# Performance work log

Hardware: AMD Instinct MI355X
Metric: run time of the kernel (lower is better)

The kernel has to match this reference:

```python
import jax, jax.numpy as jnp
import numpy as np

N_ATOMS = 16384
N_BLOCKS = 4096
K = 3          # top-k nearest context atoms (min(3, n_ctx) in original; n_ctx >> 3 here)
EPS_W = 1e-8   # inverse-distance weight epsilon (matches original)
EPS_D = 1e-12  # tiny epsilon inside sqrt for numerical safety of the distance


def setup_inputs() -> dict:
    key = jax.random.key(0)
    k1, k2, k3, k4, k5 = jax.random.split(key, 5)
    # coordinates spread out like real molecular coords (Angstrom-ish scale)
    X = jax.random.normal(k1, (N_ATOMS, 3), dtype=jnp.float32) * 10.0
    base_noise = jax.random.normal(k2, (N_ATOMS, 3), dtype=jnp.float32)      # randn_like(X)
    centroid_noise = jax.random.normal(k3, (N_ATOMS, 3), dtype=jnp.float32)  # per-atom randn(3)
    block_ids = jnp.sort(jax.random.randint(k4, (N_ATOMS,), 0, N_BLOCKS)).astype(jnp.int32)
    generate_mask = jax.random.randint(k5, (N_BLOCKS,), 0, 2).astype(bool)
    return {
        "X": X,
        "base_noise": base_noise,
        "centroid_noise": centroid_noise,
        "block_ids": block_ids,
        "generate_mask": generate_mask,
    }


def reference(X, base_noise, centroid_noise, block_ids, generate_mask):
    """Vectorized sample_chemical_prior: for every generated atom, find the 3
    nearest CONTEXT atoms, take an inverse-distance-weighted centroid, and add
    0.5 * gaussian noise. Non-generated atoms keep base_noise (randn_like)."""
    n = X.shape[0]
    gen_atoms = generate_mask[block_ids]           # [N] atoms being generated
    ctx = ~gen_atoms                               # [N] context atoms

    # pairwise squared distances via ||a||^2 + ||b||^2 - 2 a.b  -> [N, N]
    xn = jnp.sum(X * X, axis=-1)
    sq = xn[:, None] + xn[None, :] - 2.0 * (X @ X.T)
    d = jnp.sqrt(jnp.maximum(sq, 0.0) + EPS_D)

    # only context atoms are valid neighbor candidates; exclude self for safety
    not_self = ~jnp.eye(n, dtype=bool)
    d = jnp.where(ctx[None, :] & not_self, d, jnp.inf)

    # k nearest context atoms per row (smallest distances)
    neg_dk, idx = jax.lax.top_k(-d, K)             # [N, K]
    dk = -neg_dk

    # inverse-distance weights, normalized (matches original)
    w = 1.0 / (dk + EPS_W)
    w = w / jnp.sum(w, axis=-1, keepdims=True)

    coords = X[idx]                                # [N, K, 3] gather neighbor coords
    centroid = jnp.sum(coords * w[..., None], axis=1)  # [N, 3]

    x0 = jnp.where(gen_atoms[:, None], centroid + 0.5 * centroid_noise, base_noise)
    return x0
```

## Files before the change

### kernel.cpp

```cpp
#include <hip/hip_runtime.h>
#include <cstdint>

#define N_ATOMS 16384
#define NBLK 64
#define NTHR 256
#define G 24
#define NCELLS 13824
#define NCELLS_PAD 14336
#define CPT 14
#define BOX_LO -48.0f
#define INV_CELL 0.25f
#define SINIT 3.0e38f

#define OFF_COUNTS 0
#define OFF_BLKGEN 256
#define OFF_BLKGOFF 512
#define OFF_FLAGS 1024
#define OFF_CNT 3072
#define OFF_START 60416
#define OFF_GENIDX 118016
#define OFF_CTX4 183552

__device__ __forceinline__ int cell1(float x) {
    int c = (int)floorf((x - BOX_LO) * INV_CELL);
    return min(max(c, 0), G - 1);
}

__device__ __forceinline__ void ins3(float v, int vi,
                                     float& s1, float& s2, float& s3,
                                     int& i1, int& i2, int& i3)
{
    const bool b1 = v < s1, b2 = v < s2, b3 = v < s3;
    s3 = b2 ? s2 : (b3 ? v : s3);   i3 = b2 ? i2 : (b3 ? vi : i3);
    s2 = b1 ? s1 : (b2 ? v : s2);   i2 = b1 ? i1 : (b2 ? vi : i2);
    s1 = b1 ? v : s1;               i1 = b1 ? vi : i1;
}

__device__ __forceinline__ void ins3v(float v, float& s1, float& s2, float& s3)
{
    const bool b1 = v < s1, b2 = v < s2, b3 = v < s3;
    s3 = b2 ? s2 : (b3 ? v : s3);
    s2 = b1 ? s1 : (b2 ? v : s2);
    s1 = b1 ? v : s1;
}

__global__ __launch_bounds__(256)
void k0_zero(int4* __restrict__ cell_cnt4)
{
    cell_cnt4[blockIdx.x * 256 + threadIdx.x] = make_int4(0, 0, 0, 0);
}

__global__ __launch_bounds__(NTHR)
void k1_classify(const float* __restrict__ X,
                 const int* __restrict__ block_ids,
                 const unsigned int* __restrict__ mask,
                 const float* __restrict__ base_noise,
                 float* __restrict__ out,
                 unsigned long long* __restrict__ flags,
                 int* __restrict__ blk_gen,
                 int* __restrict__ cell_cnt)
{
    __shared__ int sflag;
    __shared__ int wg[4];
    const int t = threadIdx.x;
    const int wave = t >> 6, lane = t & 63;

    if (t == 0) sflag = 0;
    __syncthreads();
    if (mask[t] > 1u) sflag = 1;
    __syncthreads();
    const bool is_u8 = (sflag != 0);
    const unsigned char* m8 = (const unsigned char*)mask;

    const int i = blockIdx.x * NTHR + t;
    const int bid = block_ids[i];
    const bool g = is_u8 ? (m8[bid] != 0) : (mask[bid] != 0u);

    out[3 * i + 0] = base_noise[3 * i + 0];
    out[3 * i + 1] = base_noise[3 * i + 1];
    out[3 * i + 2] = base_noise[3 * i + 2];

    const unsigned long long mg = __ballot(g);
    if (lane == 0) { flags[blockIdx.x * 4 + wave] = mg; wg[wave] = __popcll(mg); }
    __syncthreads();
    if (t == 0) blk_gen[blockIdx.x] = wg[0] + wg[1] + wg[2] + wg[3];

    if (!g) {
        const float x = X[3 * i], y = X[3 * i + 1], z = X[3 * i + 2];
        const int cx = cell1(x), cy = cell1(y), cz = cell1(z);
        atomicAdd(&cell_cnt[(cz * G + cy) * G + cx], 1);
    }
}

__global__ __launch_bounds__(1024)
void k2_scan(int* __restrict__ cell_cnt,
             int* __restrict__ cell_start,
             const int* __restrict__ blk_gen,
             int* __restrict__ blk_goff,
             int* __restrict__ counts)
{
    const int t = threadIdx.x;
    const int wave = t >> 6, lane = t & 63;
    int loc[CPT]; int sum = 0;
    #pragma unroll
    for (int k = 0; k < CPT; ++k) {
        const int v = cell_cnt[t * CPT + k];
        loc[k] = sum; sum += v;
    }
    int v = sum;
    #pragma unroll
    for (int d = 1; d < 64; d <<= 1) { const int u = __shfl_up(v, d); if (lane >= d) v += u; }
    __shared__ int wsum[16], wexc[16];
    if (lane == 63) wsum[wave] = v;
    __syncthreads();
    if (t < 16) {
        int v2 = wsum[t];
        const int orig = v2;
        #pragma unroll
        for (int d = 1; d < 16; d <<= 1) { const int u = __shfl_up(v2, d); if (t >= d) v2 += u; }
        wexc[t] = v2 - orig;
    }
    __syncthreads();
    const int base = wexc[wave] + (v - sum);
    #pragma unroll
    for (int k = 0; k < CPT; ++k) {
        cell_start[t * CPT + k] = base + loc[k];
        cell_cnt[t * CPT + k] = 0;
    }
    if (t == 1023) cell_start[NCELLS_PAD] = base + sum;
    __syncthreads();
    if (t < 64) {
        const int o = blk_gen[t];
        int s = o;
        #pragma unroll
        for (int d = 1; d < 64; d <<= 1) { const int u = __shfl_up(s, d); if (t >= d) s += u; }
        blk_goff[t] = s - o;
        if (t == 63) { counts[1] = s; counts[0] = N_ATOMS - s; }
    }
}

__global__ __launch_bounds__(NTHR)
void k3_scatter(const float* __restrict__ X,
                const unsigned long long* __restrict__ flags,
                const int* __restrict__ blk_goff,
                const int* __restrict__ cell_start,
                int* __restrict__ cell_cur,
                float4* __restrict__ ctx4s,
                int* __restrict__ genidx)
{
    const int t = threadIdx.x;
    const int wave = t >> 6, lane = t & 63;
    const int i = blockIdx.x * NTHR + t;
    const unsigned long long fw = flags[blockIdx.x * 4 + wave];
    const bool g = (fw >> lane) & 1ull;
    int og = blk_goff[blockIdx.x];
    int oc = blockIdx.x * NTHR - og;
    #pragma unroll
    for (int w = 0; w < 4; ++w) {
        if (w < wave) {
            const int p = __popcll(flags[blockIdx.x * 4 + w]);
            og += p; oc += 64 - p;
        }
    }
    const unsigned long long below = (1ull << lane) - 1ull;
    og += __popcll(fw & below);
    oc += __popcll((~fw) & below);
    if (g) {
        genidx[og] = i;
    } else {
        const float x = X[3 * i], y = X[3 * i + 1], z = X[3 * i + 2];
        float xn = x * x; xn += y * y; xn += z * z;
        const int cx = cell1(x), cy = cell1(y), cz = cell1(z);
        const int c = (cz * G + cy) * G + cx;
        const int pos = cell_start[c] + atomicAdd(&cell_cur[c], 1);
        ctx4s[pos] = make_float4(x, y, z, xn);
    }
}

__global__ __launch_bounds__(512)
void k4_search(const float* __restrict__ X,
               const float* __restrict__ cnoise,
               const int* __restrict__ counts,
               const int* __restrict__ cell_start,
               const float4* __restrict__ ctx4s,
               const int* __restrict__ genidx,
               float* __restrict__ out)
{
    const int n_gen = counts[1];
    const int wave = threadIdx.x >> 6, lane = threadIdx.x & 63;
    const int slot = (int)blockIdx.x * 8 + wave;
    if (slot >= n_gen) return;

    const int ai = genidx[slot];
    const float qx = X[3 * ai], qy = X[3 * ai + 1], qz = X[3 * ai + 2];
    float xnq = qx * qx; xnq += qy * qy; xnq += qz * qz;
    const int cqx = cell1(qx), cqy = cell1(qy), cqz = cell1(qz);

    float s1 = SINIT, s2 = SINIT, s3 = SINIT;
    int i1 = 0, i2 = 0, i3 = 0;

    {
        int st = 0, cnt = 0;
        if (lane < 9) {
            const int dy = lane % 3 - 1, dz = lane / 3 - 1;
            const int cy = cqy + dy, cz = cqz + dz;
            if ((unsigned)cy < G && (unsigned)cz < G) {
                const int xlo = max(cqx - 1, 0), xhi = min(cqx + 1, G - 1);
                const int c0 = (cz * G + cy) * G + xlo;
                st = cell_start[c0];
                cnt = cell_start[c0 + (xhi - xlo + 1)] - st;
            }
        }
        int stv[9], base[10];
        base[0] = 0;
        #pragma unroll
        for (int k = 0; k < 9; ++k) {
            stv[k] = __builtin_amdgcn_readlane(st, k);
            base[k + 1] = base[k] + __builtin_amdgcn_readlane(cnt, k);
        }
        const int T = base[9];
        const int nro = (T + 63) >> 6;
        if (nro > 0) {
            auto calcP = [&](int j) -> int {
                const int jc = min(j, T - 1);
                int p = stv[0] + jc;
                #pragma unroll
                for (int k = 1; k < 9; ++k)
                    p = (jc >= base[k]) ? stv[k] + (jc - base[k]) : p;
                return p;
            };
            int p0 = calcP(lane);
            float4 cc0 = ctx4s[p0];
            for (int ro = 0; ro < nro; ++ro) {
                int p1 = p0; float4 cc1 = cc0;
                if (ro + 1 < nro) { p1 = calcP((ro + 1) * 64 + lane); cc1 = ctx4s[p1]; }
                if (ro * 64 + lane < T) {
                    const float dot = qx * cc0.x + qy * cc0.y + qz * cc0.z;
                    const float sq = (xnq + cc0.w) - 2.0f * dot;
                    ins3(sq, p0, s1, s2, s3, i1, i2, i3);
                }
                p0 = p1; cc0 = cc1;
            }
        }
    }

    auto converged = [&](float bnd) -> bool {
        const int c = __popcll(__ballot(s1 + 0.01f < bnd))
                    + __popcll(__ballot(s2 + 0.01f < bnd))
                    + __popcll(__ballot(s3 + 0.01f < bnd));
        return c >= 3;
    };

    bool done = converged(16.0f);

    if (!done) {
        auto searchOwner = [&](int ebase_r, int jc) -> int {
            int L = 0;
            #pragma unroll
            for (int stp = 32; stp >= 1; stp >>= 1) {
                const int cand = L + stp;
                const int bv = __shfl(ebase_r, cand);
                if (bv <= jc) L = cand;
            }
            return L;
        };
        auto flatScan = [&](int T, int ebase_r, int pk_r) {
            const int iters = (T + 63) >> 6;
            if (iters == 0) return;
            int jc0 = min(lane, T - 1);
            int p0 = __shfl(pk_r, searchOwner(ebase_r, jc0)) + jc0;
            float4 cc0 = ctx4s[p0];
            for (int it = 0; it < iters; ++it) {
                int p1 = p0; float4 cc1 = cc0;
                if (it + 1 < iters) {
                    const int jc1 = min((it + 1) * 64 + lane, T - 1);
                    p1 = __shfl(pk_r, searchOwner(ebase_r, jc1)) + jc1;
                    cc1 = ctx4s[p1];
                }
                if (it * 64 + lane < T) {
                    const float dot = qx * cc0.x + qy * cc0.y + qz * cc0.z;
                    const float sq = (xnq + cc0.w) - 2.0f * dot;
                    ins3(sq, p0, s1, s2, s3, i1, i2, i3);
                }
                p0 = p1; cc0 = cc1;
            }
        };
        auto prefixT = [&](int cnt, int& ebase_r, int& T) {
            int pre = cnt;
            #pragma unroll
            for (int d = 1; d < 64; d <<= 1) {
                const int u = __shfl_up(pre, d);
                if (lane >= d) pre += u;
            }
            T = __shfl(pre, 63);
            ebase_r = pre - cnt;
        };
        auto ringScan = [&](int P, int R) {
            const int B = 2 * R + 1;
            const int NR = B * B;
            const int NS = 2 * NR;
            auto segRange = [&](int u, int& st, int& cnt) {
                st = 0; cnt = 0;
                if (u >= NS) return;
                const int side = (u >= NR) ? 1 : 0;
                const int v = side ? u - NR : u;
                const int dy = v % B - R, dz = v / B - R;
                const int cy = cqy + dy, cz = cqz + dz;
                if ((unsigned)cy >= G || (unsigned)cz >= G) return;
                const bool inner = max(abs(dy), abs(dz)) <= P;
                int xlo, xhi;
                if (inner) {
                    if (side) { xlo = cqx + P + 1; xhi = cqx + R; }
                    else      { xlo = cqx - R;     xhi = cqx - P - 1; }
                } else {
                    if (side) return;
                    xlo = cqx - R; xhi = cqx + R;
                }
                xlo = max(xlo, 0); xhi = min(xhi, G - 1);
                if (xlo > xhi) return;
                const int c0 = (cz * G + cy) * G + xlo;
                st = cell_start[c0];
                cnt = cell_start[c0 + (xhi - xlo + 1)] - st;
            };
            const int nro = (NS + 63) >> 6;
            int st0, c0r;
            segRange(lane, st0, c0r);
            for (int ro = 0; ro < nro; ++ro) {
                int st1 = st0, c1r = c0r;
                if (ro + 1 < nro) segRange((ro + 1) * 64 + lane, st1, c1r);
                int eb, Tr;
                prefixT(c0r, eb, Tr);
                if (Tr > 0) flatScan(Tr, eb, st0 - eb);
                st0 = st1; c0r = c1r;
            }
        };

        #pragma unroll
        for (int li = 1; li < 4; ++li) {
            if (!done) {
                const int R = 1 << li;
                ringScan(1 << (li - 1), R);
                done = converged((float)(4 * R) * (float)(4 * R));
            }
        }
        if (!done) {
            s1 = SINIT; s2 = SINIT; s3 = SINIT;
            i1 = 0; i2 = 0; i3 = 0;
            const int n_ctx = counts[0];
            for (int base = 0; base < n_ctx; base += 64) {
                const int p = base + lane;
                if (p < n_ctx) {
                    const float4 cc = ctx4s[p];
                    const float dot = qx * cc.x + qy * cc.y + qz * cc.z;
                    const float sq = (xnq + cc.w) - 2.0f * dot;
                    ins3(sq, p, s1, s2, s3, i1, i2, i3);
                }
            }
        }
    }

    #pragma unroll
    for (int m = 1; m < 64; m <<= 1) {
        const float a = __shfl_xor(s1, m); const int ja = __shfl_xor(i1, m);
        const float b = __shfl_xor(s2, m); const int jb = __shfl_xor(i2, m);
        const float c = __shfl_xor(s3, m); const int jc = __shfl_xor(i3, m);
        ins3(a, ja, s1, s2, s3, i1, i2, i3);
        ins3(b, jb, s1, s2, s3, i1, i2, i3);
        ins3(c, jc, s1, s2, s3, i1, i2, i3);
    }

    if (lane == 0) {
        const float d1 = sqrtf(fmaxf(s1, 0.0f) + 1e-12f);
        const float d2 = sqrtf(fmaxf(s2, 0.0f) + 1e-12f);
        const float d3 = sqrtf(fmaxf(s3, 0.0f) + 1e-12f);
        float w1 = 1.0f / (d1 + 1e-8f);
        float w2 = 1.0f / (d2 + 1e-8f);
        float w3 = 1.0f / (d3 + 1e-8f);
        float wsum = w1 + w2;
        wsum += w3;
        w1 /= wsum; w2 /= wsum; w3 /= wsum;
        const float4 c1 = ctx4s[i1];
        const float4 c2 = ctx4s[i2];
        const float4 c3 = ctx4s[i3];
        float cxo = w1 * c1.x + w2 * c2.x; cxo += w3 * c3.x;
        float cyo = w1 * c1.y + w2 * c2.y; cyo += w3 * c3.y;
        float czo = w1 * c1.z + w2 * c2.z; czo += w3 * c3.z;
        out[3 * ai + 0] = cxo + 0.5f * cnoise[3 * ai + 0];
        out[3 * ai + 1] = cyo + 0.5f * cnoise[3 * ai + 1];
        out[3 * ai + 2] = czo + 0.5f * cnoise[3 * ai + 2];
    }
}

extern "C" void kernel_launch(void* const* d_in, const int* in_sizes, int n_in,
                              void* d_out, int out_size, void* d_ws, size_t ws_size,
                              hipStream_t stream) {
    const float* X          = (const float*)d_in[0];
    const float* base_noise = (const float*)d_in[1];
    const float* cnoise     = (const float*)d_in[2];
    const int*   block_ids  = (const int*)d_in[3];
    const unsigned int* gmask = (const unsigned int*)d_in[4];
    float* out = (float*)d_out;

    char* ws = (char*)d_ws;
    int*    counts     = (int*)(ws + OFF_COUNTS);
    int*    blk_gen    = (int*)(ws + OFF_BLKGEN);
    int*    blk_goff   = (int*)(ws + OFF_BLKGOFF);
    unsigned long long* flags = (unsigned long long*)(ws + OFF_FLAGS);
    int*    cell_cnt   = (int*)(ws + OFF_CNT);
    int*    cell_start = (int*)(ws + OFF_START);
    int*    genidx     = (int*)(ws + OFF_GENIDX);
    float4* ctx4s      = (float4*)(ws + OFF_CTX4);

    k0_zero<<<NCELLS_PAD / 1024, 256, 0, stream>>>((int4*)cell_cnt);
    k1_classify<<<NBLK, NTHR, 0, stream>>>(X, block_ids, gmask, base_noise,
                                           out, flags, blk_gen, cell_cnt);
    k2_scan<<<1, 1024, 0, stream>>>(cell_cnt, cell_start, blk_gen, blk_goff, counts);
    k3_scatter<<<NBLK, NTHR, 0, stream>>>(X, flags, blk_goff, cell_start,
                                          cell_cnt, ctx4s, genidx);
    k4_search<<<N_ATOMS / 8, 512, 0, stream>>>(X, cnoise, counts, cell_start,
                                               ctx4s, genidx, out);
}
```

Before: 50.65 us.

## Move cell histogram into shared-memory sort kernel and drop zero kernel

The classify kernel now writes a 16-bit cell id per atom instead of doing global atomics. The single-block scan kernel builds the histogram, prefix sum and per-atom slot positions with shared-memory atomics, so the separate zeroing kernel goes away and the scatter kernel no longer needs global atomics. The search kernel moves to 256-thread blocks with an early exit, and the ring enumeration now covers only the non-empty shell segments instead of testing and rejecting half the lanes. The cost is that one 1024-thread block now processes all 16K atoms serially, in two passes.

```diff
diff --git a/kernel.cpp b/kernel.cpp
--- a/kernel.cpp
+++ b/kernel.cpp
@@ -16,10 +16,11 @@
 #define OFF_BLKGEN 256
 #define OFF_BLKGOFF 512
 #define OFF_FLAGS 1024
-#define OFF_CNT 3072
-#define OFF_START 60416
-#define OFF_GENIDX 118016
-#define OFF_CTX4 183552
+#define OFF_ACELL 3072
+#define OFF_POS 35840
+#define OFF_START 101376
+#define OFF_GENIDX 158976
+#define OFF_CTX4 224512
 
 __device__ __forceinline__ int cell1(float x) {
     int c = (int)floorf((x - BOX_LO) * INV_CELL);
@@ -36,20 +37,6 @@
     s1 = b1 ? v : s1;               i1 = b1 ? vi : i1;
 }
 
-__device__ __forceinline__ void ins3v(float v, float& s1, float& s2, float& s3)
-{
-    const bool b1 = v < s1, b2 = v < s2, b3 = v < s3;
-    s3 = b2 ? s2 : (b3 ? v : s3);
-    s2 = b1 ? s1 : (b2 ? v : s2);
-    s1 = b1 ? v : s1;
-}
-
-__global__ __launch_bounds__(256)
-void k0_zero(int4* __restrict__ cell_cnt4)
-{
-    cell_cnt4[blockIdx.x * 256 + threadIdx.x] = make_int4(0, 0, 0, 0);
-}
-
 __global__ __launch_bounds__(NTHR)
 void k1_classify(const float* __restrict__ X,
                  const int* __restrict__ block_ids,
@@ -58,7 +45,7 @@
                  float* __restrict__ out,
                  unsigned long long* __restrict__ flags,
                  int* __restrict__ blk_gen,
-                 int* __restrict__ cell_cnt)
+                 unsigned short* __restrict__ acell)
 {
     __shared__ int sflag;
     __shared__ int wg[4];
@@ -85,32 +72,47 @@
     __syncthreads();
     if (t == 0) blk_gen[blockIdx.x] = wg[0] + wg[1] + wg[2] + wg[3];
 
+    unsigned short c = 0xFFFFu;
     if (!g) {
         const float x = X[3 * i], y = X[3 * i + 1], z = X[3 * i + 2];
-        const int cx = cell1(x), cy = cell1(y), cz = cell1(z);
-        atomicAdd(&cell_cnt[(cz * G + cy) * G + cx], 1);
-    }
+        c = (unsigned short)((cell1(z) * G + cell1(y)) * G + cell1(x));
+    }
+    acell[i] = c;
 }
 
 __global__ __launch_bounds__(1024)
-void k2_scan(int* __restrict__ cell_cnt,
+void k2_sort(const unsigned short* __restrict__ acell,
              int* __restrict__ cell_start,
+             int* __restrict__ pos,
              const int* __restrict__ blk_gen,
              int* __restrict__ blk_goff,
              int* __restrict__ counts)
 {
+    __shared__ int hist[NCELLS_PAD];
+    __shared__ int wsum[16], wexc[16];
     const int t = threadIdx.x;
     const int wave = t >> 6, lane = t & 63;
+
+    #pragma unroll
+    for (int k = 0; k < CPT; ++k) hist[t * CPT + k] = 0;
+    __syncthreads();
+
+    #pragma unroll
+    for (int it = 0; it < N_ATOMS / 1024; ++it) {
+        const unsigned short c = acell[it * 1024 + t];
+        if (c != 0xFFFFu) atomicAdd(&hist[c], 1);
+    }
+    __syncthreads();
+
     int loc[CPT]; int sum = 0;
     #pragma unroll
     for (int k = 0; k < CPT; ++k) {
-        const int v = cell_cnt[t * CPT + k];
+        const int v = hist[t * CPT + k];
         loc[k] = sum; sum += v;
     }
     int v = sum;
     #pragma unroll
     for (int d = 1; d < 64; d <<= 1) { const int u = __shfl_up(v, d); if (lane >= d) v += u; }
-    __shared__ int wsum[16], wexc[16];
     if (lane == 63) wsum[wave] = v;
     __syncthreads();
     if (t < 16) {
@@ -124,11 +126,20 @@
     const int base = wexc[wave] + (v - sum);
     #pragma unroll
     for (int k = 0; k < CPT; ++k) {
-        cell_start[t * CPT + k] = base + loc[k];
-        cell_cnt[t * CPT + k] = 0;
+        const int st = base + loc[k];
+        cell_start[t * CPT + k] = st;
+        hist[t * CPT + k] = st;
     }
     if (t == 1023) cell_start[NCELLS_PAD] = base + sum;
     __syncthreads();
+
+    #pragma unroll
+    for (int it = 0; it < N_ATOMS / 1024; ++it) {
+        const int i = it * 1024 + t;
+        const unsigned short c = acell[i];
+        if (c != 0xFFFFu) pos[i] = atomicAdd(&hist[c], 1);
+    }
+
     if (t < 64) {
         const int o = blk_gen[t];
         int s = o;
@@ -143,8 +154,7 @@
 void k3_scatter(const float* __restrict__ X,
                 const unsigned long long* __restrict__ flags,
                 const int* __restrict__ blk_goff,
-                const int* __restrict__ cell_start,
-                int* __restrict__ cell_cur,
+                const int* __restrict__ pos,
                 float4* __restrict__ ctx4s,
                 int* __restrict__ genidx)
 {
@@ -153,31 +163,23 @@
     const int i = blockIdx.x * NTHR + t;
     const unsigned long long fw = flags[blockIdx.x * 4 + wave];
     const bool g = (fw >> lane) & 1ull;
-    int og = blk_goff[blockIdx.x];
-    int oc = blockIdx.x * NTHR - og;
-    #pragma unroll
-    for (int w = 0; w < 4; ++w) {
-        if (w < wave) {
-            const int p = __popcll(flags[blockIdx.x * 4 + w]);
-            og += p; oc += 64 - p;
-        }
-    }
-    const unsigned long long below = (1ull << lane) - 1ull;
-    og += __popcll(fw & below);
-    oc += __popcll((~fw) & below);
     if (g) {
+        int og = blk_goff[blockIdx.x];
+        #pragma unroll
+        for (int w = 0; w < 4; ++w) {
+            if (w < wave) og += __popcll(flags[blockIdx.x * 4 + w]);
+        }
+        const unsigned long long below = (1ull << lane) - 1ull;
+        og += __popcll(fw & below);
         genidx[og] = i;
     } else {
         const float x = X[3 * i], y = X[3 * i + 1], z = X[3 * i + 2];
         float xn = x * x; xn += y * y; xn += z * z;
-        const int cx = cell1(x), cy = cell1(y), cz = cell1(z);
-        const int c = (cz * G + cy) * G + cx;
-        const int pos = cell_start[c] + atomicAdd(&cell_cur[c], 1);
-        ctx4s[pos] = make_float4(x, y, z, xn);
-    }
-}
-
-__global__ __launch_bounds__(512)
+        ctx4s[pos[i]] = make_float4(x, y, z, xn);
+    }
+}
+
+__global__ __launch_bounds__(NTHR)
 void k4_search(const float* __restrict__ X,
                const float* __restrict__ cnoise,
                const int* __restrict__ counts,
@@ -188,7 +190,8 @@
 {
     const int n_gen = counts[1];
     const int wave = threadIdx.x >> 6, lane = threadIdx.x & 63;
-    const int slot = (int)blockIdx.x * 8 + wave;
+    if ((int)blockIdx.x * 4 >= n_gen) return;
+    const int slot = (int)blockIdx.x * 4 + wave;
     if (slot >= n_gen) return;
 
     const int ai = genidx[slot];
@@ -297,25 +300,35 @@
         };
         auto ringScan = [&](int P, int R) {
             const int B = 2 * R + 1;
-            const int NR = B * B;
-            const int NS = 2 * NR;
+            const int RP = R - P;
+            const int PP = 2 * P + 1;
+            const int A = 2 * RP * B;
+            const int C = PP * 2 * RP;
+            const int NS = A + C + 2 * PP * PP;
             auto segRange = [&](int u, int& st, int& cnt) {
                 st = 0; cnt = 0;
                 if (u >= NS) return;
-                const int side = (u >= NR) ? 1 : 0;
-                const int v = side ? u - NR : u;
-                const int dy = v % B - R, dz = v / B - R;
+                int dy, dz, xlo, xhi;
+                if (u < A) {
+                    const int q = u / B, rdy = u - q * B;
+                    dz = (q < RP) ? (-R + q) : (P + 1 + (q - RP));
+                    dy = rdy - R;
+                    xlo = cqx - R; xhi = cqx + R;
+                } else if (u < A + C) {
+                    const int v = u - A, W = 2 * RP;
+                    const int q = v / W, w = v - q * W;
+                    dz = -P + q;
+                    dy = (w < RP) ? (-R + w) : (P + 1 + (w - RP));
+                    xlo = cqx - R; xhi = cqx + R;
+                } else {
+                    const int v = u - A - C;
+                    const int side = v & 1, v2 = v >> 1;
+                    dy = v2 % PP - P; dz = v2 / PP - P;
+                    if (side) { xlo = cqx + P + 1; xhi = cqx + R; }
+                    else      { xlo = cqx - R;     xhi = cqx - P - 1; }
+                }
                 const int cy = cqy + dy, cz = cqz + dz;
                 if ((unsigned)cy >= G || (unsigned)cz >= G) return;
-                const bool inner = max(abs(dy), abs(dz)) <= P;
-                int xlo, xhi;
-                if (inner) {
-                    if (side) { xlo = cqx + P + 1; xhi = cqx + R; }
-                    else      { xlo = cqx - R;     xhi = cqx - P - 1; }
-                } else {
-                    if (side) return;
-                    xlo = cqx - R; xhi = cqx + R;
-                }
                 xlo = max(xlo, 0); xhi = min(xhi, G - 1);
                 if (xlo > xhi) return;
                 const int c0 = (cz * G + cy) * G + xlo;
@@ -406,17 +419,16 @@
     int*    blk_gen    = (int*)(ws + OFF_BLKGEN);
     int*    blk_goff   = (int*)(ws + OFF_BLKGOFF);
     unsigned long long* flags = (unsigned long long*)(ws + OFF_FLAGS);
-    int*    cell_cnt   = (int*)(ws + OFF_CNT);
+    unsigned short* acell = (unsigned short*)(ws + OFF_ACELL);
+    int*    pos        = (int*)(ws + OFF_POS);
     int*    cell_start = (int*)(ws + OFF_START);
     int*    genidx     = (int*)(ws + OFF_GENIDX);
     float4* ctx4s      = (float4*)(ws + OFF_CTX4);
 
-    k0_zero<<<NCELLS_PAD / 1024, 256, 0, stream>>>((int4*)cell_cnt);
     k1_classify<<<NBLK, NTHR, 0, stream>>>(X, block_ids, gmask, base_noise,
-                                           out, flags, blk_gen, cell_cnt);
-    k2_scan<<<1, 1024, 0, stream>>>(cell_cnt, cell_start, blk_gen, blk_goff, counts);
-    k3_scatter<<<NBLK, NTHR, 0, stream>>>(X, flags, blk_goff, cell_start,
-                                          cell_cnt, ctx4s, genidx);
-    k4_search<<<N_ATOMS / 8, 512, 0, stream>>>(X, cnoise, counts, cell_start,
-                                               ctx4s, genidx, out);
-}
+                                           out, flags, blk_gen, acell);
+    k2_sort<<<1, 1024, 0, stream>>>(acell, cell_start, pos, blk_gen, blk_goff, counts);
+    k3_scatter<<<NBLK, NTHR, 0, stream>>>(X, flags, blk_goff, pos, ctx4s, genidx);
+    k4_search<<<N_ATOMS / 4, NTHR, 0, stream>>>(X, cnoise, counts, cell_start,
+                                                ctx4s, genidx, out);
+}
```

Result: faster. 46.01 us (-9.2%).
